# Kernel tuning notes

Measured on AMD Instinct MI355X. Metric: run time of the kernel, lower is better.

## Reference

```python
import jax, jax.numpy as jnp
import numpy as np

B, S, D, H = 2, 2048, 1024, 16
DK = D // H

def setup_inputs() -> dict:
    key = jax.random.key(0)
    ks = jax.random.split(key, 9)
    scale = 1.0 / np.sqrt(D)
    return {
        "x": jax.random.normal(ks[0], (B, S, D), dtype=jnp.float32),
        "Wq": jax.random.uniform(ks[1], (D, D), jnp.float32, -scale, scale),
        "bq": jax.random.uniform(ks[2], (D,), jnp.float32, -scale, scale),
        "Wk": jax.random.uniform(ks[3], (D, D), jnp.float32, -scale, scale),
        "bk": jax.random.uniform(ks[4], (D,), jnp.float32, -scale, scale),
        "Wv": jax.random.uniform(ks[5], (D, D), jnp.float32, -scale, scale),
        "bv": jax.random.uniform(ks[6], (D,), jnp.float32, -scale, scale),
        "Wo": jax.random.uniform(ks[7], (D, D), jnp.float32, -scale, scale),
        "bo": jax.random.uniform(ks[8], (D,), jnp.float32, -scale, scale),
    }

def reference(x, Wq, bq, Wk, bk, Wv, bv, Wo, bo):
    # QKV projections (torch Linear: x @ W.T + b)
    q = x @ Wq.T + bq
    k = x @ Wk.T + bk
    v = x @ Wv.T + bv
    # [B, H, S, DK]
    q = q.reshape(B, S, H, DK).transpose(0, 2, 1, 3)
    k = k.reshape(B, S, H, DK).transpose(0, 2, 1, 3)
    v = v.reshape(B, S, H, DK).transpose(0, 2, 1, 3)
    scores = jnp.einsum('bhqd,bhkd->bhqk', q, k) / jnp.sqrt(jnp.float32(DK))
    p = jax.nn.softmax(scores, axis=-1)  # dropout is identity in eval mode
    o = jnp.einsum('bhqk,bhkd->bhqd', p, v)
    o = o.transpose(0, 2, 1, 3).reshape(B, S, D)
    return o @ Wo.T + bo
```

## Files before the change

### kernel.cpp

```cpp
#include <hip/hip_runtime.h>


typedef __attribute__((ext_vector_type(8))) short short8;
typedef __attribute__((ext_vector_type(4))) short short4v;
typedef __attribute__((ext_vector_type(4))) float f32x4;
typedef __attribute__((ext_vector_type(8))) unsigned short u16x8;
typedef __attribute__((ext_vector_type(2))) unsigned int u32x2;

__device__ __forceinline__ unsigned short f2bf(float f) {
    unsigned int u = __builtin_bit_cast(unsigned int, f);
    u += 0x7FFFu + ((u >> 16) & 1u);
    return (unsigned short)(u >> 16);
}

__device__ __forceinline__ float exp2_fast(float x) {
    return __builtin_amdgcn_exp2f(x);
}

__device__ __forceinline__ void gload16(const void* gsrc, void* ldst) {
    __builtin_amdgcn_global_load_lds(
        (const __attribute__((address_space(1))) unsigned int*)gsrc,
        (__attribute__((address_space(3))) unsigned int*)ldst, 16, 0, 0);
}

__global__ void cast_all(const float* __restrict__ x,
                         const float* __restrict__ wq, const float* __restrict__ wk,
                         const float* __restrict__ wv, const float* __restrict__ wo,
                         unsigned short* __restrict__ xb,
                         unsigned short* __restrict__ wqb, unsigned short* __restrict__ wkb,
                         unsigned short* __restrict__ wvb, unsigned short* __restrict__ wob)
{
    const int z = blockIdx.y;
    const float* src; unsigned short* dst; int n4;
    if (z == 0)      { src = x;  dst = xb;  n4 = 4096 * 1024 / 4; }
    else if (z == 1) { src = wq; dst = wqb; n4 = 1024 * 1024 / 4; }
    else if (z == 2) { src = wk; dst = wkb; n4 = 1024 * 1024 / 4; }
    else if (z == 3) { src = wv; dst = wvb; n4 = 1024 * 1024 / 4; }
    else             { src = wo; dst = wob; n4 = 1024 * 1024 / 4; }
    int i = blockIdx.x * blockDim.x + threadIdx.x;
    if (i < n4) {
        float4 v = reinterpret_cast<const float4*>(src)[i];
        ushort4 o;
        o.x = f2bf(v.x); o.y = f2bf(v.y); o.z = f2bf(v.z); o.w = f2bf(v.w);
        reinterpret_cast<ushort4*>(dst)[i] = o;
    }
}

__global__ __launch_bounds__(256, 2)
void qkv_gemm(const unsigned short* __restrict__ A,
              const unsigned short* __restrict__ Wq_,
              const unsigned short* __restrict__ Wk_,
              const unsigned short* __restrict__ Wv_,
              const float* __restrict__ bq_,
              const float* __restrict__ bk_,
              const float* __restrict__ bv_,
              unsigned short* __restrict__ Qb,
              unsigned short* __restrict__ Kb,
              unsigned short* __restrict__ Vtb)
{
    const int K = 1024;
    __shared__ __align__(16) unsigned short As[128][64];
    __shared__ __align__(16) unsigned short Bs[128][64];

    const int z = blockIdx.z;
    const unsigned short* Bw = (z == 0) ? Wq_ : (z == 1) ? Wk_ : Wv_;
    const float* bias = (z == 0) ? bq_ : (z == 1) ? bk_ : bv_;
    unsigned short* dst = (z == 0) ? Qb : (z == 1) ? Kb : Vtb;
    const float alpha = (z == 0) ? 0.125f * 1.44269504088896340736f : 1.0f;

    const int tid  = threadIdx.x;
    const int lane = tid & 63;
    const int wave = tid >> 6;
    const int wm = (wave >> 1) * 64;
    const int wn = (wave & 1) * 64;
    const int rowBase = blockIdx.y * 128;
    const int colBase = blockIdx.x * 128;
    const int l15 = lane & 15;
    const int lg  = lane >> 4;

    const int srow   = lane >> 3;
    const int schunk = lane & 7;
    const int gchunk = schunk ^ srow;

    f32x4 acc[4][4] = {};

    for (int kt = 0; kt < K; kt += 64) {
        __syncthreads();
#pragma unroll
        for (int it = 0; it < 4; ++it) {
            int r = wave * 8 + it * 32 + srow;
            gload16(A  + (size_t)(rowBase + r) * K + kt + gchunk * 8, &As[wave * 8 + it * 32][0]);
            gload16(Bw + (size_t)(colBase + r) * K + kt + gchunk * 8, &Bs[wave * 8 + it * 32][0]);
        }
        __syncthreads();
#pragma unroll
        for (int kk = 0; kk < 2; ++kk) {
            short8 af[4], bf[4];
#pragma unroll
            for (int fm = 0; fm < 4; ++fm) {
                int r  = wm + fm * 16 + l15;
                int kb = (kk * 4 + lg) ^ (r & 7);
                af[fm] = *reinterpret_cast<const short8*>(&As[r][kb * 8]);
            }
#pragma unroll
            for (int fn = 0; fn < 4; ++fn) {
                int r  = wn + fn * 16 + l15;
                int kb = (kk * 4 + lg) ^ (r & 7);
                bf[fn] = *reinterpret_cast<const short8*>(&Bs[r][kb * 8]);
            }
#pragma unroll
            for (int fm = 0; fm < 4; ++fm)
#pragma unroll
                for (int fn = 0; fn < 4; ++fn)
                    acc[fm][fn] = __builtin_amdgcn_mfma_f32_16x16x32_bf16(
                        af[fm], bf[fn], acc[fm][fn], 0, 0, 0);
        }
    }

#pragma unroll
    for (int fm = 0; fm < 4; ++fm)
#pragma unroll
        for (int fn = 0; fn < 4; ++fn)
#pragma unroll
            for (int r = 0; r < 4; ++r) {
                int grow = rowBase + wm + fm * 16 + lg * 4 + r;
                int gcol = colBase + wn + fn * 16 + l15;
                float v = (acc[fm][fn][r] + bias[gcol]) * alpha;
                int b = grow >> 11, s = grow & 2047;
                int h = gcol >> 6,  dk = gcol & 63;
                if (z < 2)
                    dst[(((size_t)b * 16 + h) * 2048 + s) * 64 + dk] = f2bf(v);
                else
                    dst[(((size_t)b * 16 + h) * 64 + dk) * 2048 + s] = f2bf(v);
            }
}

__global__ __launch_bounds__(256, 2)
void gemm_out(const unsigned short* __restrict__ A,
              const unsigned short* __restrict__ Bw,
              const float* __restrict__ bias,
              float* __restrict__ Cout, int M, int N, int K)
{
    __shared__ __align__(16) unsigned short As[128][64];
    __shared__ __align__(16) unsigned short Bs[128][64];

    const int tid  = threadIdx.x;
    const int lane = tid & 63;
    const int wave = tid >> 6;
    const int wm = (wave >> 1) * 64;
    const int wn = (wave & 1) * 64;
    const int rowBase = blockIdx.y * 128;
    const int colBase = blockIdx.x * 128;
    const int l15 = lane & 15;
    const int lg  = lane >> 4;

    const int srow   = lane >> 3;
    const int schunk = lane & 7;
    const int gchunk = schunk ^ srow;

    f32x4 acc[4][4] = {};

    for (int kt = 0; kt < K; kt += 64) {
        __syncthreads();
#pragma unroll
        for (int it = 0; it < 4; ++it) {
            int r = wave * 8 + it * 32 + srow;
            gload16(A  + (size_t)(rowBase + r) * K + kt + gchunk * 8, &As[wave * 8 + it * 32][0]);
            gload16(Bw + (size_t)(colBase + r) * K + kt + gchunk * 8, &Bs[wave * 8 + it * 32][0]);
        }
        __syncthreads();
#pragma unroll
        for (int kk = 0; kk < 2; ++kk) {
            short8 af[4], bf[4];
#pragma unroll
            for (int fm = 0; fm < 4; ++fm) {
                int r  = wm + fm * 16 + l15;
                int kb = (kk * 4 + lg) ^ (r & 7);
                af[fm] = *reinterpret_cast<const short8*>(&As[r][kb * 8]);
            }
#pragma unroll
            for (int fn = 0; fn < 4; ++fn) {
                int r  = wn + fn * 16 + l15;
                int kb = (kk * 4 + lg) ^ (r & 7);
                bf[fn] = *reinterpret_cast<const short8*>(&Bs[r][kb * 8]);
            }
#pragma unroll
            for (int fm = 0; fm < 4; ++fm)
#pragma unroll
                for (int fn = 0; fn < 4; ++fn)
                    acc[fm][fn] = __builtin_amdgcn_mfma_f32_16x16x32_bf16(
                        af[fm], bf[fn], acc[fm][fn], 0, 0, 0);
        }
    }

#pragma unroll
    for (int fm = 0; fm < 4; ++fm)
#pragma unroll
        for (int fn = 0; fn < 4; ++fn)
#pragma unroll
            for (int r = 0; r < 4; ++r) {
                int grow = rowBase + wm + fm * 16 + lg * 4 + r;
                int gcol = colBase + wn + fn * 16 + l15;
                Cout[(size_t)grow * N + gcol] = acc[fm][fn][r] + bias[gcol];
            }
}

__global__ __launch_bounds__(256, 2)
void attn_kernel(const unsigned short* __restrict__ Q,
                 const unsigned short* __restrict__ Kt,
                 const unsigned short* __restrict__ Vt,
                 unsigned short* __restrict__ O)
{
    __shared__ __align__(16) unsigned short Ks[128][64];
    __shared__ __align__(16) unsigned short Vs[64][128];
    __shared__ __align__(16) unsigned short Ps[4][32][64];

    const int bh = blockIdx.y;
    const int qt = blockIdx.x;
    const int tid  = threadIdx.x;
    const int lane = tid & 63;
    const int w    = tid >> 6;
    const int l15 = lane & 15;
    const int lg  = lane >> 4;

    const unsigned short* Qbh = Q  + (size_t)bh * 2048 * 64;
    const unsigned short* Kbh = Kt + (size_t)bh * 2048 * 64;
    const unsigned short* Vbh = Vt + (size_t)bh * 64 * 2048;

    short8 qf[2][2];
#pragma unroll
    for (int fq = 0; fq < 2; ++fq)
#pragma unroll
        for (int kk = 0; kk < 2; ++kk) {
            int row = qt * 128 + w * 32 + fq * 16 + l15;
            qf[fq][kk] = *reinterpret_cast<const short8*>(
                Qbh + (size_t)row * 64 + kk * 32 + lg * 8);
        }

    float mst[2] = {-1e30f, -1e30f};
    float lst[2] = {0.f, 0.f};
    f32x4 accO[2][4] = {};

    const int sr  = tid >> 3, skb = tid & 7;
    const int vr  = tid >> 4, vkb = tid & 15;

    unsigned short* PsW = &Ps[w][0][0];

    u16x8 kst[4], vst[4];
#pragma unroll
    for (int it = 0; it < 4; ++it)
        kst[it] = *reinterpret_cast<const u16x8*>(Kbh + (size_t)(sr + it * 32) * 64 + skb * 8);
#pragma unroll
    for (int it = 0; it < 4; ++it)
        vst[it] = *reinterpret_cast<const u16x8*>(Vbh + (size_t)(vr + it * 16) * 2048 + vkb * 8);

    for (int t = 0; t < 16; ++t) {
        __syncthreads();
#pragma unroll
        for (int it = 0; it < 4; ++it) {
            int r = sr + it * 32;
            *reinterpret_cast<u16x8*>(&Ks[r][(skb ^ (r & 7)) * 8]) = kst[it];
        }
#pragma unroll
        for (int it = 0; it < 4; ++it) {
            int r = vr + it * 16;
            *reinterpret_cast<u16x8*>(&Vs[r][(vkb ^ (r & 15)) * 8]) = vst[it];
        }
        __syncthreads();

        if (t < 15) {
#pragma unroll
            for (int it = 0; it < 4; ++it)
                kst[it] = *reinterpret_cast<const u16x8*>(
                    Kbh + (size_t)((t + 1) * 128 + sr + it * 32) * 64 + skb * 8);
#pragma unroll
            for (int it = 0; it < 4; ++it)
                vst[it] = *reinterpret_cast<const u16x8*>(
                    Vbh + (size_t)(vr + it * 16) * 2048 + (t + 1) * 128 + vkb * 8);
        }

        f32x4 accS[8][2] = {};
#pragma unroll
        for (int kk = 0; kk < 2; ++kk) {
            short8 kf[8];
#pragma unroll
            for (int fk = 0; fk < 8; ++fk) {
                int r  = fk * 16 + l15;
                int kb = (kk * 4 + lg) ^ (r & 7);
                kf[fk] = *reinterpret_cast<const short8*>(&Ks[r][kb * 8]);
            }
#pragma unroll
            for (int fk = 0; fk < 8; ++fk)
#pragma unroll
                for (int fq = 0; fq < 2; ++fq)
                    accS[fk][fq] = __builtin_amdgcn_mfma_f32_16x16x32_bf16(
                        kf[fk], qf[fq][kk], accS[fk][fq], 0, 0, 0);
        }

        float newms[2], psums[2] = {0.f, 0.f};
#pragma unroll
        for (int fq = 0; fq < 2; ++fq) {
            float mx = -1e30f;
#pragma unroll
            for (int fk = 0; fk < 8; ++fk)
#pragma unroll
                for (int r = 0; r < 4; ++r) mx = fmaxf(mx, accS[fk][fq][r]);
            mx = fmaxf(mx, __shfl_xor(mx, 16));
            mx = fmaxf(mx, __shfl_xor(mx, 32));
            float newm = fmaxf(mst[fq], mx);
            float corr = exp2_fast(mst[fq] - newm);
            mst[fq] = newm; newms[fq] = newm;
            lst[fq] *= corr;
#pragma unroll
            for (int r = 0; r < 4; ++r) {
                float cq = __shfl(corr, lg * 4 + r);
#pragma unroll
                for (int fd = 0; fd < 4; ++fd) accO[fq][fd][r] *= cq;
            }
        }

#pragma unroll
        for (int hh = 0; hh < 2; ++hh) {
#pragma unroll
            for (int fq = 0; fq < 2; ++fq) {
                const int ql = fq * 16 + l15;
#pragma unroll
                for (int f2 = 0; f2 < 4; ++f2) {
                    int fk = hh * 4 + f2;
                    float p0 = exp2_fast(accS[fk][fq][0] - newms[fq]);
                    float p1 = exp2_fast(accS[fk][fq][1] - newms[fq]);
                    float p2 = exp2_fast(accS[fk][fq][2] - newms[fq]);
                    float p3 = exp2_fast(accS[fk][fq][3] - newms[fq]);
                    psums[fq] += (p0 + p1) + (p2 + p3);
                    unsigned int lo = (unsigned int)f2bf(p0) | ((unsigned int)f2bf(p1) << 16);
                    unsigned int hi = (unsigned int)f2bf(p2) | ((unsigned int)f2bf(p3) << 16);
                    u32x2 tmp; tmp.x = lo; tmp.y = hi;
                    short4v pk = __builtin_bit_cast(short4v, tmp);
                    int c = (f2 * 2 + (lg >> 1)) ^ (ql & 7);
                    *reinterpret_cast<short4v*>(
                        reinterpret_cast<char*>(PsW) + ql * 128 + c * 16 + (lg & 1) * 8) = pk;
                }
            }
            asm volatile("" ::: "memory");

#pragma unroll
            for (int k2 = 0; k2 < 2; ++k2) {
                short8 pf[2], vf[4];
#pragma unroll
                for (int fq = 0; fq < 2; ++fq) {
                    int ql = fq * 16 + l15;
                    int c  = (k2 * 4 + lg) ^ (ql & 7);
                    pf[fq] = *reinterpret_cast<const short8*>(
                        reinterpret_cast<char*>(PsW) + ql * 128 + c * 16);
                }
#pragma unroll
                for (int fd = 0; fd < 4; ++fd) {
                    int row = fd * 16 + l15;
                    int kb  = ((hh * 2 + k2) * 4 + lg) ^ (row & 15);
                    vf[fd] = *reinterpret_cast<const short8*>(&Vs[row][kb * 8]);
                }
#pragma unroll
                for (int fq = 0; fq < 2; ++fq)
#pragma unroll
                    for (int fd = 0; fd < 4; ++fd)
                        accO[fq][fd] = __builtin_amdgcn_mfma_f32_16x16x32_bf16(
                            pf[fq], vf[fd], accO[fq][fd], 0, 0, 0);
            }
            asm volatile("" ::: "memory");
        }

#pragma unroll
        for (int fq = 0; fq < 2; ++fq) {
            float ps = psums[fq];
            ps += __shfl_xor(ps, 16);
            ps += __shfl_xor(ps, 32);
            lst[fq] += ps;
        }
    }

    const int b = bh >> 4, h = bh & 15;
#pragma unroll
    for (int fq = 0; fq < 2; ++fq)
#pragma unroll
        for (int r = 0; r < 4; ++r) {
            float linv = 1.0f / __shfl(lst[fq], lg * 4 + r);
            int s = qt * 128 + w * 32 + fq * 16 + lg * 4 + r;
#pragma unroll
            for (int fd = 0; fd < 4; ++fd) {
                int dk = fd * 16 + l15;
                O[((size_t)b * 2048 + s) * 1024 + h * 64 + dk] = f2bf(accO[fq][fd][r] * linv);
            }
        }
}

extern "C" void kernel_launch(void* const* d_in, const int* in_sizes, int n_in,
                              void* d_out, int out_size, void* d_ws, size_t ws_size,
                              hipStream_t stream)
{
    const float* x  = (const float*)d_in[0];
    const float* Wq = (const float*)d_in[1];
    const float* bq = (const float*)d_in[2];
    const float* Wk = (const float*)d_in[3];
    const float* bk = (const float*)d_in[4];
    const float* Wv = (const float*)d_in[5];
    const float* bv = (const float*)d_in[6];
    const float* Wo = (const float*)d_in[7];
    const float* bo = (const float*)d_in[8];
    float* out = (float*)d_out;

    char* ws = (char*)d_ws;
    unsigned short* xb  = (unsigned short*)(ws);
    unsigned short* wqb = (unsigned short*)(ws + ((size_t)8  << 20));
    unsigned short* wkb = (unsigned short*)(ws + ((size_t)10 << 20));
    unsigned short* wvb = (unsigned short*)(ws + ((size_t)12 << 20));
    unsigned short* wob = (unsigned short*)(ws + ((size_t)14 << 20));
    unsigned short* Qb  = (unsigned short*)(ws + ((size_t)16 << 20));
    unsigned short* Kb  = (unsigned short*)(ws + ((size_t)24 << 20));
    unsigned short* Vtb = (unsigned short*)(ws + ((size_t)32 << 20));
    unsigned short* Ob  = (unsigned short*)(ws + ((size_t)40 << 20));

    cast_all<<<dim3(4096, 5), 256, 0, stream>>>(x, Wq, Wk, Wv, Wo,
                                                xb, wqb, wkb, wvb, wob);

    qkv_gemm<<<dim3(8, 32, 3), 256, 0, stream>>>(xb, wqb, wkb, wvb, bq, bk, bv,
                                                 Qb, Kb, Vtb);

    attn_kernel<<<dim3(16, 32), 256, 0, stream>>>(Qb, Kb, Vtb, Ob);

    gemm_out<<<dim3(8, 32), 256, 0, stream>>>(Ob, wob, bo, out, 4096, 1024, 1024);
}
```

Baseline: 131.0 us.

## Double-buffer K/V tiles in LDS using direct global-to-LDS async loads

The attention kernel now keeps two K and two V tiles in shared memory and prefetches the next tile straight into LDS with global_load_lds. This replaces the old register staging followed by an explicit LDS store. It removes one barrier per iteration and the register pressure of the staging buffers, so loads can overlap with the MFMA work. The cost is doubled LDS for K/V, which may lower occupancy. The swizzle is also now applied on the global-address side rather than in the LDS store.

```diff
diff --git a/kernel.cpp b/kernel.cpp
--- a/kernel.cpp
+++ b/kernel.cpp
@@ -211,8 +211,8 @@
                  const unsigned short* __restrict__ Vt,
                  unsigned short* __restrict__ O)
 {
-    __shared__ __align__(16) unsigned short Ks[128][64];
-    __shared__ __align__(16) unsigned short Vs[64][128];
+    __shared__ __align__(16) unsigned short Ks[2][128][64];
+    __shared__ __align__(16) unsigned short Vs[2][64][128];
     __shared__ __align__(16) unsigned short Ps[4][32][64];
 
     const int bh = blockIdx.y;
@@ -227,6 +227,9 @@
     const unsigned short* Kbh = Kt + (size_t)bh * 2048 * 64;
     const unsigned short* Vbh = Vt + (size_t)bh * 64 * 2048;
 
+    const int klrow = lane >> 3;
+    const int kgc   = (lane & 7) ^ klrow;
+    const int vlrow = lane >> 4;
     short8 qf[2][2];
 #pragma unroll
     for (int fq = 0; fq < 2; ++fq)
@@ -241,42 +244,33 @@
     float lst[2] = {0.f, 0.f};
     f32x4 accO[2][4] = {};
 
-    const int sr  = tid >> 3, skb = tid & 7;
-    const int vr  = tid >> 4, vkb = tid & 15;
-
     unsigned short* PsW = &Ps[w][0][0];
 
-    u16x8 kst[4], vst[4];
-#pragma unroll
-    for (int it = 0; it < 4; ++it)
-        kst[it] = *reinterpret_cast<const u16x8*>(Kbh + (size_t)(sr + it * 32) * 64 + skb * 8);
-#pragma unroll
-    for (int it = 0; it < 4; ++it)
-        vst[it] = *reinterpret_cast<const u16x8*>(Vbh + (size_t)(vr + it * 16) * 2048 + vkb * 8);
-
+#define STAGE_KV(buf, t)                                                          \
+    {                                                                             \
+        _Pragma("unroll")                                                         \
+        for (int it = 0; it < 4; ++it) {                                          \
+            int rb = it * 32 + w * 8;                                             \
+            gload16(Kbh + (size_t)((t) * 128 + rb + klrow) * 64 + kgc * 8,        \
+                    &Ks[buf][rb][0]);                                             \
+        }                                                                         \
+        _Pragma("unroll")                                                         \
+        for (int it = 0; it < 4; ++it) {                                          \
+            int rb = it * 16 + w * 4;                                             \
+            int rv = rb + vlrow;                                                  \
+            int vgc = (lane & 15) ^ (rv & 15);                                    \
+            gload16(Vbh + (size_t)rv * 2048 + (t) * 128 + vgc * 8,                \
+                    &Vs[buf][rb][0]);                                             \
+        }                                                                         \
+    }
+
+    STAGE_KV(0, 0);
+    __syncthreads();
+
+    int cur = 0;
     for (int t = 0; t < 16; ++t) {
-        __syncthreads();
-#pragma unroll
-        for (int it = 0; it < 4; ++it) {
-            int r = sr + it * 32;
-            *reinterpret_cast<u16x8*>(&Ks[r][(skb ^ (r & 7)) * 8]) = kst[it];
-        }
-#pragma unroll
-        for (int it = 0; it < 4; ++it) {
-            int r = vr + it * 16;
-            *reinterpret_cast<u16x8*>(&Vs[r][(vkb ^ (r & 15)) * 8]) = vst[it];
-        }
-        __syncthreads();
-
         if (t < 15) {
-#pragma unroll
-            for (int it = 0; it < 4; ++it)
-                kst[it] = *reinterpret_cast<const u16x8*>(
-                    Kbh + (size_t)((t + 1) * 128 + sr + it * 32) * 64 + skb * 8);
-#pragma unroll
-            for (int it = 0; it < 4; ++it)
-                vst[it] = *reinterpret_cast<const u16x8*>(
-                    Vbh + (size_t)(vr + it * 16) * 2048 + (t + 1) * 128 + vkb * 8);
+            STAGE_KV(cur ^ 1, t + 1);
         }
 
         f32x4 accS[8][2] = {};
@@ -287,7 +281,7 @@
             for (int fk = 0; fk < 8; ++fk) {
                 int r  = fk * 16 + l15;
                 int kb = (kk * 4 + lg) ^ (r & 7);
-                kf[fk] = *reinterpret_cast<const short8*>(&Ks[r][kb * 8]);
+                kf[fk] = *reinterpret_cast<const short8*>(&Ks[cur][r][kb * 8]);
             }
 #pragma unroll
             for (int fk = 0; fk < 8; ++fk)
@@ -357,7 +351,7 @@
                 for (int fd = 0; fd < 4; ++fd) {
                     int row = fd * 16 + l15;
                     int kb  = ((hh * 2 + k2) * 4 + lg) ^ (row & 15);
-                    vf[fd] = *reinterpret_cast<const short8*>(&Vs[row][kb * 8]);
+                    vf[fd] = *reinterpret_cast<const short8*>(&Vs[cur][row][kb * 8]);
                 }
 #pragma unroll
                 for (int fq = 0; fq < 2; ++fq)
@@ -376,7 +370,11 @@
             ps += __shfl_xor(ps, 32);
             lst[fq] += ps;
         }
+
+        __syncthreads();
+        cur ^= 1;
     }
+#undef STAGE_KV
 
     const int b = bh >> 4, h = bh & 15;
 #pragma unroll
```

After: 133.5 us. No clear change (+1.9%).
